# Kernel tuning notes

Measured on AMD Instinct MI355X. Metric: run time of the kernel, lower is better.

## Reference

```python
import jax, jax.numpy as jnp
import numpy as np

N_NODES = 100000
N_EDGES = 3200000
IN_DIM = 4
HID = 128
OUT_DIM = 4


def setup_inputs() -> dict:
    key = jax.random.key(0)
    ks = jax.random.split(key, 16)
    x = jax.random.normal(ks[0], (N_NODES, IN_DIM), dtype=jnp.float32)
    edge_index = jax.random.randint(ks[1], (2, N_EDGES), 0, N_NODES, dtype=jnp.int32)
    hidden_mask = jax.random.randint(ks[2], (N_NODES,), 0, 2) > 0
    def glorot(k, shape):
        fan_in, fan_out = shape[0], shape[1]
        s = jnp.sqrt(6.0 / (fan_in + fan_out))
        return jax.random.uniform(k, shape, jnp.float32, -s, s)
    return {
        "x": x,
        "edge_index": edge_index,
        "hidden_mask": hidden_mask,
        "W0": glorot(ks[3], (IN_DIM, HID)), "b0": jnp.zeros((HID,), jnp.float32),
        "res_W": glorot(ks[4], (IN_DIM, HID)), "res_b": jnp.zeros((HID,), jnp.float32),
        "W1": glorot(ks[5], (HID, HID)), "b1": jnp.zeros((HID,), jnp.float32),
        "W2": glorot(ks[6], (HID, HID)), "b2": jnp.zeros((HID,), jnp.float32),
        "fc_W": glorot(ks[7], (HID, OUT_DIM)), "fc_b": jnp.zeros((OUT_DIM,), jnp.float32),
    }


def _gcn_norm(edge_index, num_nodes):
    # add self loops, compute symmetric normalization (PyG GCNConv default)
    loop = jnp.arange(num_nodes, dtype=edge_index.dtype)
    src = jnp.concatenate([edge_index[0], loop])
    dst = jnp.concatenate([edge_index[1], loop])
    deg = jax.ops.segment_sum(jnp.ones_like(dst, dtype=jnp.float32), dst,
                              num_segments=num_nodes)
    dis = jnp.where(deg > 0, jax.lax.rsqrt(deg), 0.0)  # deg^{-1/2}, inf -> 0
    norm = dis[src] * dis[dst]  # [E + N]
    return src, dst, norm


def _gcn_conv(h, W, b, src, dst, norm, num_nodes):
    h = h @ W                       # [N, out]
    msg = h[src] * norm[:, None]    # gather + scale, [E+N, out]
    agg = jax.ops.segment_sum(msg, dst, num_segments=num_nodes)
    return agg + b


def reference(x, edge_index, hidden_mask, W0, b0, res_W, res_b, W1, b1, W2, b2, fc_W, fc_b):
    n = x.shape[0]
    src, dst, norm = _gcn_norm(edge_index, n)
    # mask input features (mask broadcast over 4 feature cols)
    h = jnp.where(hidden_mask[:, None], x, 0.0)
    # layer 0: in_dim != hidden -> linear residual
    out0 = _gcn_conv(h, W0, b0, src, dst, norm, n)
    h = jax.nn.relu(out0 + (h @ res_W + res_b))
    # layers 1,2: identity residual
    h = jax.nn.relu(_gcn_conv(h, W1, b1, src, dst, norm, n) + h)
    h = jax.nn.relu(_gcn_conv(h, W2, b2, src, dst, norm, n) + h)
    x_out = h @ fc_W + fc_b
    return (x_out, hidden_mask)
```

## Files before the change

### kernel.cpp

```cpp
#include <hip/hip_runtime.h>
#include <hip/hip_bf16.h>
#include <stdint.h>

#define HID 128
#define NPART 8
#define NCHUNK 256
#define MCHUNK 4096
#define LBITS 10
#define SBITS 22

__global__ void detect_mask_kernel(const unsigned char* __restrict__ p, int nbytes,
                                   int nfloat, int* __restrict__ flags) {
  int stride = blockDim.x * gridDim.x;
  for (int i = blockIdx.x * blockDim.x + threadIdx.x; i < nbytes; i += stride) {
    if ((i & 3) && p[i] != 0) { atomicOr(&flags[0], 1); break; }
  }
  const float* fp = (const float*)p;
  for (int i = blockIdx.x * blockDim.x + threadIdx.x; i < nfloat; i += stride) {
    float f = fp[i];
    if (!(f == 0.0f || f == 1.0f)) { atomicOr(&flags[1], 1); break; }
  }
}

__global__ void expand_mask_h0(const void* __restrict__ maskp, const float4* __restrict__ x4,
                               const int* __restrict__ flags, const float* __restrict__ dis,
                               float* __restrict__ maskout, float* __restrict__ cvec,
                               float4* __restrict__ h0s, int N) {
  int i = blockIdx.x * blockDim.x + threadIdx.x;
  if (i >= N) return;
  float m;
  if (flags[0] == 0)      m = (((const int*)maskp)[i] != 0) ? 1.f : 0.f;
  else if (flags[1] == 0) m = (((const float*)maskp)[i] != 0.f) ? 1.f : 0.f;
  else                    m = (((const unsigned char*)maskp)[i] != 0) ? 1.f : 0.f;
  maskout[i] = m;
  float4 xv = x4[i];
  float4 h0 = make_float4(m * xv.x, m * xv.y, m * xv.z, m * xv.w);
  float* cv = cvec + (size_t)i * 8;
  cv[4] = h0.x; cv[5] = h0.y; cv[6] = h0.z; cv[7] = h0.w;
  float d = dis[i];
  h0s[i] = make_float4(d * h0.x, d * h0.y, d * h0.z, d * h0.w);
}

__global__ void init_gcur_kernel(int* __restrict__ gcur, int n, int CAPB) {
  int i = blockIdx.x * blockDim.x + threadIdx.x;
  if (i < n) gcur[i] = i * CAPB;
}

__global__ void radixA_kernel(const int* __restrict__ src, const int* __restrict__ dst,
                              int* __restrict__ gcur, uint32_t* __restrict__ bdata,
                              int nbin, int CAPB, int E) {
  __shared__ uint32_t sv[MCHUNK];
  __shared__ uint16_t sb[MCHUNK];
  __shared__ int bcnt[1024], boff[1024], gbase[1024];
  __shared__ int wsum[4];
  int t = threadIdx.x;
  int base = blockIdx.x * MCHUNK;
  int m = E - base; if (m > MCHUNK) m = MCHUNK;
  for (int i = t; i < 1024; i += 256) bcnt[i] = 0;
  __syncthreads();
  uint32_t pk[16]; short bn[16];
#pragma unroll
  for (int j = 0; j < 16; j++) {
    int i = base + t + j * 256;
    if (i < base + m) {
      int d = __builtin_nontemporal_load(&dst[i]);
      int s = __builtin_nontemporal_load(&src[i]);
      int b = d >> LBITS;
      pk[j] = ((uint32_t)(d & ((1 << LBITS) - 1)) << SBITS) | (uint32_t)s;
      bn[j] = (short)b;
      atomicAdd(&bcnt[b], 1);
    } else bn[j] = -1;
  }
  __syncthreads();
  {
    int lane = t & 63, w = t >> 6, i0 = t * 4;
    int v0 = bcnt[i0], v1 = bcnt[i0 + 1], v2 = bcnt[i0 + 2], v3 = bcnt[i0 + 3];
    int ts = v0 + v1 + v2 + v3, sc = ts;
    for (int d = 1; d < 64; d <<= 1) { int x = __shfl_up(sc, d, 64); if (lane >= d) sc += x; }
    if (lane == 63) wsum[w] = sc;
    __syncthreads();
    int wo = 0;
    for (int k = 0; k < w; k++) wo += wsum[k];
    int excl = wo + sc - ts;
    boff[i0] = excl; boff[i0 + 1] = excl + v0;
    boff[i0 + 2] = excl + v0 + v1; boff[i0 + 3] = excl + v0 + v1 + v2;
  }
  __syncthreads();
  for (int i = t; i < nbin; i += 256) {
    int c = bcnt[i];
    gbase[i] = c ? atomicAdd(&gcur[i], c) : 0;
  }
  __syncthreads();
  for (int i = t; i < nbin; i += 256) bcnt[i] = boff[i];
  __syncthreads();
#pragma unroll
  for (int j = 0; j < 16; j++) {
    if (bn[j] >= 0) {
      int p = atomicAdd(&bcnt[bn[j]], 1);
      sv[p] = pk[j];
      sb[p] = (uint16_t)bn[j];
    }
  }
  __syncthreads();
  for (int i = t; i < m; i += 256) {
    int b = sb[i];
    int gp = gbase[b] + (i - boff[b]);
    if (gp < (b + 1) * CAPB) bdata[gp] = sv[i];
  }
}

__global__ void bucket_meta_kernel(const int* __restrict__ gcur, int* __restrict__ bstart,
                                   int nbin, int CAPB) {
  __shared__ int wsum[4];
  int t = threadIdx.x, lane = t & 63, w = t >> 6, i0 = t * 4;
  int v[4];
#pragma unroll
  for (int q = 0; q < 4; q++) {
    int i = i0 + q;
    int c = 0;
    if (i < nbin) {
      c = gcur[i] - i * CAPB;
      if (c > CAPB) c = CAPB;
    }
    v[q] = c;
  }
  int ts = v[0] + v[1] + v[2] + v[3], sc = ts;
  for (int d = 1; d < 64; d <<= 1) { int x = __shfl_up(sc, d, 64); if (lane >= d) sc += x; }
  if (lane == 63) wsum[w] = sc;
  __syncthreads();
  int wo = 0;
  for (int k = 0; k < w; k++) wo += wsum[k];
  int excl = wo + sc - ts;
  int e[4] = {excl, excl + v[0], excl + v[0] + v[1], excl + v[0] + v[1] + v[2]};
#pragma unroll
  for (int q = 0; q < 4; q++)
    if (i0 + q < nbin) bstart[i0 + q] = e[q];
  if (t == 255) bstart[nbin] = wo + sc;
}

__global__ void radixB_kernel(const uint32_t* __restrict__ bdata, const int* __restrict__ gcur,
                              const int* __restrict__ bstart, int CAPB,
                              int* __restrict__ off, float* __restrict__ dis,
                              int* __restrict__ csr, int N, int E) {
  __shared__ int cnt[1024], loff[1024];
  __shared__ int wsum[4];
  int b = blockIdx.x, t = threadIdx.x;
  int cb = gcur[b] - b * CAPB; if (cb > CAPB) cb = CAPB;
  int gb = bstart[b];
  const uint32_t* bd = bdata + (size_t)b * CAPB;
  for (int i = t; i < 1024; i += 256) cnt[i] = 0;
  __syncthreads();
  for (int i = t; i < cb; i += 256) atomicAdd(&cnt[bd[i] >> SBITS], 1);
  __syncthreads();
  {
    int lane = t & 63, w = t >> 6, i0 = t * 4;
    int v0 = cnt[i0], v1 = cnt[i0 + 1], v2 = cnt[i0 + 2], v3 = cnt[i0 + 3];
    int ts = v0 + v1 + v2 + v3, sc = ts;
    for (int d = 1; d < 64; d <<= 1) { int x = __shfl_up(sc, d, 64); if (lane >= d) sc += x; }
    if (lane == 63) wsum[w] = sc;
    __syncthreads();
    int wo = 0;
    for (int k = 0; k < w; k++) wo += wsum[k];
    int e0 = wo + sc - ts;
    int e1 = e0 + v0, e2 = e1 + v1, e3 = e2 + v2;
    loff[i0] = e0; loff[i0 + 1] = e1; loff[i0 + 2] = e2; loff[i0 + 3] = e3;
    int d0 = b * 1024 + i0;
    if (d0 + 0 < N) { off[d0 + 0] = gb + e0; dis[d0 + 0] = rsqrtf((float)v0 + 1.0f); }
    if (d0 + 1 < N) { off[d0 + 1] = gb + e1; dis[d0 + 1] = rsqrtf((float)v1 + 1.0f); }
    if (d0 + 2 < N) { off[d0 + 2] = gb + e2; dis[d0 + 2] = rsqrtf((float)v2 + 1.0f); }
    if (d0 + 3 < N) { off[d0 + 3] = gb + e3; dis[d0 + 3] = rsqrtf((float)v3 + 1.0f); }
  }
  if (b == 0 && t == 0) off[N] = E;
  __syncthreads();
  for (int i = t; i < 1024; i += 256) cnt[i] = loff[i];
  __syncthreads();
  for (int i = t; i < cb; i += 256) {
    uint32_t v = bd[i];
    int p = atomicAdd(&cnt[v >> SBITS], 1);
    csr[gb + p] = (int)(v & ((1u << SBITS) - 1));
  }
}

__global__ void scan1_kernel(const int* __restrict__ cnt, int* __restrict__ off,
                             int* __restrict__ bsum, float* __restrict__ dis, int N) {
  __shared__ int wsum[4];
  int t = threadIdx.x, lane = t & 63, w = t >> 6;
  int base = blockIdx.x * 1024 + t * 4;
  int v0 = (base + 0 < N) ? cnt[base + 0] : 0;
  int v1 = (base + 1 < N) ? cnt[base + 1] : 0;
  int v2 = (base + 2 < N) ? cnt[base + 2] : 0;
  int v3 = (base + 3 < N) ? cnt[base + 3] : 0;
  if (dis) {
    if (base + 0 < N) dis[base + 0] = rsqrtf((float)v0 + 1.0f);
    if (base + 1 < N) dis[base + 1] = rsqrtf((float)v1 + 1.0f);
    if (base + 2 < N) dis[base + 2] = rsqrtf((float)v2 + 1.0f);
    if (base + 3 < N) dis[base + 3] = rsqrtf((float)v3 + 1.0f);
  }
  int ts = v0 + v1 + v2 + v3;
  int sc = ts;
  for (int d = 1; d < 64; d <<= 1) {
    int x = __shfl_up(sc, d, 64);
    if (lane >= d) sc += x;
  }
  if (lane == 63) wsum[w] = sc;
  __syncthreads();
  int wo = 0;
  for (int i = 0; i < w; i++) wo += wsum[i];
  int excl = wo + sc - ts;
  if (base + 0 < N) off[base + 0] = excl;
  if (base + 1 < N) off[base + 1] = excl + v0;
  if (base + 2 < N) off[base + 2] = excl + v0 + v1;
  if (base + 3 < N) off[base + 3] = excl + v0 + v1 + v2;
  if (t == 255) bsum[blockIdx.x] = wo + sc;
}

__global__ void scan2_kernel(int* __restrict__ bsum, int nb) {
  if (threadIdx.x == 0 && blockIdx.x == 0) {
    int run = 0;
    for (int i = 0; i < nb; i++) { int v = bsum[i]; bsum[i] = run; run += v; }
  }
}

__global__ void scan3_kernel(int* __restrict__ off, const int* __restrict__ bsum,
                             int* __restrict__ cur, int N, int E) {
  int i = blockIdx.x * blockDim.x + threadIdx.x;
  if (i < N) {
    int o = off[i] + bsum[i >> 10];
    off[i] = o;
    if (cur) cur[i] = o;
  }
  if (i == 0) off[N] = E;
}

__global__ void hist_part_kernel(const int* __restrict__ dst, int* __restrict__ cnt,
                                 int E, int N) {
  int p = blockIdx.x & (NPART - 1);
  int chunk = blockIdx.x >> 3;
  int lo = (int)((long long)p * N / NPART);
  int hi = (int)((long long)(p + 1) * N / NPART);
  int stride = NCHUNK * 256;
  for (int e = chunk * 256 + threadIdx.x; e < E; e += stride) {
    int d = __builtin_nontemporal_load(&dst[e]);
    if (d >= lo && d < hi) atomicAdd(&cnt[d], 1);
  }
}

__global__ void fill_part_kernel(const int* __restrict__ src, const int* __restrict__ dst,
                                 int* __restrict__ cur, int* __restrict__ csr, int E, int N) {
  int p = blockIdx.x & (NPART - 1);
  int chunk = blockIdx.x >> 3;
  int lo = (int)((long long)p * N / NPART);
  int hi = (int)((long long)(p + 1) * N / NPART);
  int stride = NCHUNK * 256;
  for (int e = chunk * 256 + threadIdx.x; e < E; e += stride) {
    int d = __builtin_nontemporal_load(&dst[e]);
    if (d >= lo && d < hi) {
      int s = __builtin_nontemporal_load(&src[e]);
      int pos = atomicAdd(&cur[d], 1);
      csr[pos] = s;
    }
  }
}

__global__ void l0_agg_kernel(const float4* __restrict__ h0s, const float* __restrict__ dis,
                              const int* __restrict__ off, const int* __restrict__ csr,
                              float* __restrict__ cvec, int N) {
  int n = blockIdx.x * blockDim.x + threadIdx.x;
  if (n >= N) return;
  float4 a = h0s[n];
  int e0 = off[n], e1 = off[n + 1];
  int i = e0;
  for (; i < e1 && (i & 3); i++) {
    float4 v = h0s[csr[i]];
    a.x += v.x; a.y += v.y; a.z += v.z; a.w += v.w;
  }
  for (; i + 4 <= e1; i += 4) {
    int4 c = *(const int4*)&csr[i];
    float4 v0 = h0s[c.x], v1 = h0s[c.y], v2 = h0s[c.z], v3 = h0s[c.w];
    a.x += v0.x + v1.x + v2.x + v3.x;
    a.y += v0.y + v1.y + v2.y + v3.y;
    a.z += v0.z + v1.z + v2.z + v3.z;
    a.w += v0.w + v1.w + v2.w + v3.w;
  }
  for (; i < e1; i++) {
    float4 v = h0s[csr[i]];
    a.x += v.x; a.y += v.y; a.z += v.z; a.w += v.w;
  }
  float dn = dis[n];
  float* cv = cvec + (size_t)n * 8;
  cv[0] = dn * a.x; cv[1] = dn * a.y; cv[2] = dn * a.z; cv[3] = dn * a.w;
}

__global__ void l0_combine_kernel(const float* __restrict__ cvec, const float* __restrict__ W0,
                                  const float* __restrict__ b0, const float* __restrict__ resW,
                                  const float* __restrict__ resb, const float* __restrict__ dis,
                                  float* __restrict__ h1, __hip_bfloat16* __restrict__ hbout) {
  int idx = blockIdx.x * blockDim.x + threadIdx.x;
  int n = idx >> 7, c = idx & 127;
  const float* cv = cvec + (size_t)n * 8;
  float acc = b0[c] + resb[c];
#pragma unroll
  for (int k = 0; k < 4; k++) {
    acc += cv[k] * W0[k * HID + c];
    acc += cv[4 + k] * resW[k * HID + c];
  }
  float v = fmaxf(acc, 0.0f);
  h1[idx] = v;
  if (hbout) hbout[idx] = __float2bfloat16(dis[n] * v);
}

#define ACC1(W) { a0 += __uint_as_float((W) << 16); a1 += __uint_as_float((W) & 0xffff0000u); }
__global__ void agg_hid_bf16_kernel(const uint32_t* __restrict__ hb, const float* __restrict__ dis,
                                    const int* __restrict__ off, const int* __restrict__ csr,
                                    uint32_t* __restrict__ aggout, int N) {
  int node = blockIdx.x * 4 + (threadIdx.x >> 6);
  int lane = threadIdx.x & 63;
  if (node >= N) return;
  uint32_t w = hb[(size_t)node * 64 + lane];
  float a0 = __uint_as_float(w << 16);
  float a1 = __uint_as_float(w & 0xffff0000u);
  int e0 = off[node], e1 = off[node + 1];
  int i = e0;
  for (; i < e1 && (i & 3); i++) {
    uint32_t ww = hb[(size_t)csr[i] * 64 + lane];
    ACC1(ww)
  }
  for (; i + 8 <= e1; i += 8) {
    int4 c0 = *(const int4*)&csr[i];
    int4 c1 = *(const int4*)&csr[i + 4];
    uint32_t w0 = hb[(size_t)c0.x * 64 + lane];
    uint32_t w1 = hb[(size_t)c0.y * 64 + lane];
    uint32_t w2 = hb[(size_t)c0.z * 64 + lane];
    uint32_t w3 = hb[(size_t)c0.w * 64 + lane];
    uint32_t w4 = hb[(size_t)c1.x * 64 + lane];
    uint32_t w5 = hb[(size_t)c1.y * 64 + lane];
    uint32_t w6 = hb[(size_t)c1.z * 64 + lane];
    uint32_t w7 = hb[(size_t)c1.w * 64 + lane];
    ACC1(w0) ACC1(w1) ACC1(w2) ACC1(w3) ACC1(w4) ACC1(w5) ACC1(w6) ACC1(w7)
  }
  for (; i + 4 <= e1; i += 4) {
    int4 c = *(const int4*)&csr[i];
    uint32_t w0 = hb[(size_t)c.x * 64 + lane];
    uint32_t w1 = hb[(size_t)c.y * 64 + lane];
    uint32_t w2 = hb[(size_t)c.z * 64 + lane];
    uint32_t w3 = hb[(size_t)c.w * 64 + lane];
    ACC1(w0) ACC1(w1) ACC1(w2) ACC1(w3)
  }
  for (; i < e1; i++) {
    uint32_t ww = hb[(size_t)csr[i] * 64 + lane];
    ACC1(ww)
  }
  float dn = dis[node];
  __hip_bfloat162 p = __float22bfloat162_rn(make_float2(dn * a0, dn * a1));
  aggout[(size_t)node * 64 + lane] = *(uint32_t*)&p;
}

__global__ void agg_hid_kernel(const float* __restrict__ h, const float* __restrict__ dis,
                               const int* __restrict__ off, const int* __restrict__ csr,
                               float* __restrict__ out, int N) {
  int node = blockIdx.x * 4 + (threadIdx.x >> 6);
  int lane = threadIdx.x & 63;
  if (node >= N) return;
  float dn = dis[node];
  const float* hrow = h + (size_t)node * HID;
  float a0 = dn * hrow[lane];
  float a1 = dn * hrow[lane + 64];
  int e0 = off[node], e1 = off[node + 1];
  for (int i = e0; i < e1; i++) {
    int s = csr[i];
    float d = dis[s];
    const float* hs = h + (size_t)s * HID;
    a0 += d * hs[lane];
    a1 += d * hs[lane + 64];
  }
  out[(size_t)node * HID + lane] = dn * a0;
  out[(size_t)node * HID + lane + 64] = dn * a1;
}

__global__ void gemm_resid_relu_kernel(const void* __restrict__ agp, int agBf16,
                                       float* __restrict__ hout,
                                       const float* __restrict__ hres,
                                       const float* __restrict__ W, const float* __restrict__ b,
                                       const float* __restrict__ dis,
                                       __hip_bfloat16* __restrict__ hbout, int N) {
  __shared__ float ash[64 * HID];
  int t = threadIdx.x;
  int n0 = blockIdx.x * 64;
  if (agBf16) {
    const uint32_t* agb = (const uint32_t*)agp;
    for (int i = t; i < 64 * 64; i += 256) {
      int gn = n0 + (i >> 6);
      uint32_t w = (gn < N) ? agb[(size_t)gn * 64 + (i & 63)] : 0u;
      ash[(i >> 6) * HID + (i & 63) * 2]     = __uint_as_float(w << 16);
      ash[(i >> 6) * HID + (i & 63) * 2 + 1] = __uint_as_float(w & 0xffff0000u);
    }
  } else {
    const float* agf = (const float*)agp;
    for (int i = t; i < 64 * HID; i += 256) {
      int gn = n0 + (i >> 7);
      ash[i] = (gn < N) ? agf[(size_t)gn * HID + (i & 127)] : 0.0f;
    }
  }
  __syncthreads();
  int tc = t & 31;
  int tn = t >> 5;
  float acc[8][4];
#pragma unroll
  for (int j = 0; j < 8; j++)
#pragma unroll
    for (int q = 0; q < 4; q++) acc[j][q] = 0.0f;

  for (int k = 0; k < HID; k += 4) {
    float4 w0 = *(const float4*)&W[(k + 0) * HID + tc * 4];
    float4 w1 = *(const float4*)&W[(k + 1) * HID + tc * 4];
    float4 w2 = *(const float4*)&W[(k + 2) * HID + tc * 4];
    float4 w3 = *(const float4*)&W[(k + 3) * HID + tc * 4];
#pragma unroll
    for (int j = 0; j < 8; j++) {
      float4 a = *(const float4*)&ash[(tn * 8 + j) * HID + k];
      acc[j][0] += a.x * w0.x + a.y * w1.x + a.z * w2.x + a.w * w3.x;
      acc[j][1] += a.x * w0.y + a.y * w1.y + a.z * w2.y + a.w * w3.y;
      acc[j][2] += a.x * w0.z + a.y * w1.z + a.z * w2.z + a.w * w3.z;
      acc[j][3] += a.x * w0.w + a.y * w1.w + a.z * w2.w + a.w * w3.w;
    }
  }
  float4 bv = *(const float4*)&b[tc * 4];
#pragma unroll
  for (int j = 0; j < 8; j++) {
    int gn = n0 + tn * 8 + j;
    if (gn < N) {
      float4 hv = *(const float4*)&hres[(size_t)gn * HID + tc * 4];
      float4 o;
      o.x = fmaxf(acc[j][0] + bv.x + hv.x, 0.0f);
      o.y = fmaxf(acc[j][1] + bv.y + hv.y, 0.0f);
      o.z = fmaxf(acc[j][2] + bv.z + hv.z, 0.0f);
      o.w = fmaxf(acc[j][3] + bv.w + hv.w, 0.0f);
      *(float4*)&hout[(size_t)gn * HID + tc * 4] = o;
      if (hbout) {
        float dnn = dis[gn];
        __hip_bfloat162 p01 = __float22bfloat162_rn(make_float2(dnn * o.x, dnn * o.y));
        __hip_bfloat162 p23 = __float22bfloat162_rn(make_float2(dnn * o.z, dnn * o.w));
        *(__hip_bfloat162*)&hbout[(size_t)gn * HID + tc * 4] = p01;
        *(__hip_bfloat162*)&hbout[(size_t)gn * HID + tc * 4 + 2] = p23;
      }
    }
  }
}

__global__ void gemm_resid_fc_kernel(const void* __restrict__ agp, int agBf16,
                                     const float* __restrict__ hres,
                                     const float* __restrict__ W, const float* __restrict__ b,
                                     const float* __restrict__ fcW, const float* __restrict__ fcb,
                                     float* __restrict__ out, int N) {
  __shared__ float ash[64 * HID];
  int t = threadIdx.x;
  int n0 = blockIdx.x * 64;
  if (agBf16) {
    const uint32_t* agb = (const uint32_t*)agp;
    for (int i = t; i < 64 * 64; i += 256) {
      int gn = n0 + (i >> 6);
      uint32_t w = (gn < N) ? agb[(size_t)gn * 64 + (i & 63)] : 0u;
      ash[(i >> 6) * HID + (i & 63) * 2]     = __uint_as_float(w << 16);
      ash[(i >> 6) * HID + (i & 63) * 2 + 1] = __uint_as_float(w & 0xffff0000u);
    }
  } else {
    const float* agf = (const float*)agp;
    for (int i = t; i < 64 * HID; i += 256) {
      int gn = n0 + (i >> 7);
      ash[i] = (gn < N) ? agf[(size_t)gn * HID + (i & 127)] : 0.0f;
    }
  }
  __syncthreads();
  int tc = t & 31;
  int tn = t >> 5;
  float acc[8][4];
#pragma unroll
  for (int j = 0; j < 8; j++)
#pragma unroll
    for (int q = 0; q < 4; q++) acc[j][q] = 0.0f;

  for (int k = 0; k < HID; k += 4) {
    float4 w0 = *(const float4*)&W[(k + 0) * HID + tc * 4];
    float4 w1 = *(const float4*)&W[(k + 1) * HID + tc * 4];
    float4 w2 = *(const float4*)&W[(k + 2) * HID + tc * 4];
    float4 w3 = *(const float4*)&W[(k + 3) * HID + tc * 4];
#pragma unroll
    for (int j = 0; j < 8; j++) {
      float4 a = *(const float4*)&ash[(tn * 8 + j) * HID + k];
      acc[j][0] += a.x * w0.x + a.y * w1.x + a.z * w2.x + a.w * w3.x;
      acc[j][1] += a.x * w0.y + a.y * w1.y + a.z * w2.y + a.w * w3.y;
      acc[j][2] += a.x * w0.z + a.y * w1.z + a.z * w2.z + a.w * w3.z;
      acc[j][3] += a.x * w0.w + a.y * w1.w + a.z * w2.w + a.w * w3.w;
    }
  }
  float4 f0 = *(const float4*)&fcW[(tc * 4 + 0) * 4];
  float4 f1 = *(const float4*)&fcW[(tc * 4 + 1) * 4];
  float4 f2 = *(const float4*)&fcW[(tc * 4 + 2) * 4];
  float4 f3 = *(const float4*)&fcW[(tc * 4 + 3) * 4];
  float4 bv = *(const float4*)&b[tc * 4];
  float4 fb = *(const float4*)&fcb[0];
#pragma unroll
  for (int j = 0; j < 8; j++) {
    int gn = n0 + tn * 8 + j;
    float4 o = make_float4(0.f, 0.f, 0.f, 0.f);
    if (gn < N) {
      float4 hv = *(const float4*)&hres[(size_t)gn * HID + tc * 4];
      o.x = fmaxf(acc[j][0] + bv.x + hv.x, 0.0f);
      o.y = fmaxf(acc[j][1] + bv.y + hv.y, 0.0f);
      o.z = fmaxf(acc[j][2] + bv.z + hv.z, 0.0f);
      o.w = fmaxf(acc[j][3] + bv.w + hv.w, 0.0f);
    }
    float r0 = o.x * f0.x + o.y * f1.x + o.z * f2.x + o.w * f3.x;
    float r1 = o.x * f0.y + o.y * f1.y + o.z * f2.y + o.w * f3.y;
    float r2 = o.x * f0.z + o.y * f1.z + o.z * f2.z + o.w * f3.z;
    float r3 = o.x * f0.w + o.y * f1.w + o.z * f2.w + o.w * f3.w;
#pragma unroll
    for (int d = 1; d < 32; d <<= 1) {
      r0 += __shfl_xor(r0, d, 64);
      r1 += __shfl_xor(r1, d, 64);
      r2 += __shfl_xor(r2, d, 64);
      r3 += __shfl_xor(r3, d, 64);
    }
    if (tc == 0 && gn < N)
      *(float4*)&out[(size_t)gn * 4] =
          make_float4(r0 + fb.x, r1 + fb.y, r2 + fb.z, r3 + fb.w);
  }
}

extern "C" void kernel_launch(void* const* d_in, const int* in_sizes, int n_in,
                              void* d_out, int out_size, void* d_ws, size_t ws_size,
                              hipStream_t stream) {
  const float* x = (const float*)d_in[0];
  const int* edge = (const int*)d_in[1];
  const void* maskp = d_in[2];
  const float* W0 = (const float*)d_in[3];
  const float* b0 = (const float*)d_in[4];
  const float* resW = (const float*)d_in[5];
  const float* resb = (const float*)d_in[6];
  const float* W1 = (const float*)d_in[7];
  const float* b1 = (const float*)d_in[8];
  const float* W2 = (const float*)d_in[9];
  const float* b2 = (const float*)d_in[10];
  const float* fcW = (const float*)d_in[11];
  const float* fcb = (const float*)d_in[12];
  float* out = (float*)d_out;

  int N = in_sizes[0] / 4;
  int E = in_sizes[1] / 2;
  const int* srcp = edge;
  const int* dstp = edge + E;

  char* ws = (char*)d_ws;
  size_t cursor = 0;
  auto alloc = [&](size_t bytes) { char* p = ws + cursor; cursor += (bytes + 511) & ~(size_t)511; return p; };
  int* flags = (int*)alloc(16);
  int* cnt = (int*)alloc((size_t)N * 4);
  float* dis = (float*)alloc((size_t)N * 4);
  int* off = (int*)alloc((size_t)(N + 1) * 4);
  int* bsum = (int*)alloc(1024);
  int nbin = (N + 1023) >> 10;
  int* gcur = (int*)alloc((size_t)(nbin + 1) * 4);
  int* bstart = (int*)alloc((size_t)(nbin + 1) * 4);
  int* csr = (int*)alloc((size_t)E * 4);
  float* h0s = (float*)alloc((size_t)N * 4 * 4);
  float* cvec = (float*)alloc((size_t)N * 8 * 4);
  float* buf0 = (float*)alloc((size_t)N * HID * 4);
  float* buf1 = (float*)alloc((size_t)N * HID * 4);
  size_t base_cursor = cursor;
  __hip_bfloat16* hb = (__hip_bfloat16*)alloc((size_t)N * HID * 2);
  uint32_t* aggbf = (uint32_t*)alloc((size_t)N * 64 * 4);
  bool use_bf16 = (cursor <= ws_size);
  if (!use_bf16) {
    hb = nullptr;
    aggbf = nullptr;
    if (base_cursor > ws_size) return;
  }

  long long expect = (long long)E / (nbin > 0 ? nbin : 1);
  int CAPB = (int)((((expect * 5) / 4 + 127) / 64) * 64);
  if (CAPB < 256) CAPB = 256;
  size_t bdata_bytes = (size_t)nbin * CAPB * 4;
  bool use_radix = (N <= (1 << SBITS)) && (nbin <= 1024) &&
                   (bdata_bytes <= (size_t)N * HID * 4);
  uint32_t* bdata = (uint32_t*)buf1;

  int nThreadsN = (N + 255) / 256;

  hipMemsetAsync(flags, 0, 16, stream);
  detect_mask_kernel<<<256, 256, 0, stream>>>((const unsigned char*)maskp, N, N / 4, flags);

  if (use_radix) {
    init_gcur_kernel<<<(nbin + 255) / 256, 256, 0, stream>>>(gcur, nbin, CAPB);
    radixA_kernel<<<(E + MCHUNK - 1) / MCHUNK, 256, 0, stream>>>(srcp, dstp, gcur, bdata,
                                                                 nbin, CAPB, E);
    bucket_meta_kernel<<<1, 256, 0, stream>>>(gcur, bstart, nbin, CAPB);
    radixB_kernel<<<nbin, 256, 0, stream>>>(bdata, gcur, bstart, CAPB, off, dis, csr, N, E);
  } else {
    hipMemsetAsync(cnt, 0, (size_t)N * 4, stream);
    int nb = (N + 1023) / 1024;
    hist_part_kernel<<<NPART * NCHUNK, 256, 0, stream>>>(dstp, cnt, E, N);
    scan1_kernel<<<nb, 256, 0, stream>>>(cnt, off, bsum, dis, N);
    scan2_kernel<<<1, 64, 0, stream>>>(bsum, nb);
    scan3_kernel<<<nThreadsN, 256, 0, stream>>>(off, bsum, cnt, N, E);
    fill_part_kernel<<<NPART * NCHUNK, 256, 0, stream>>>(srcp, dstp, cnt, csr, E, N);
  }

  expand_mask_h0<<<nThreadsN, 256, 0, stream>>>(maskp, (const float4*)x, flags, dis,
                                                out + (size_t)N * 4, cvec, (float4*)h0s, N);

  l0_agg_kernel<<<nThreadsN, 256, 0, stream>>>((const float4*)h0s, dis, off, csr, cvec, N);
  l0_combine_kernel<<<(N * HID + 255) / 256, 256, 0, stream>>>(cvec, W0, b0, resW, resb, dis,
                                                               buf0, hb);

  if (use_bf16) {
    agg_hid_bf16_kernel<<<(N + 3) / 4, 256, 0, stream>>>((const uint32_t*)hb, dis, off, csr,
                                                         aggbf, N);
    gemm_resid_relu_kernel<<<(N + 63) / 64, 256, 0, stream>>>(aggbf, 1, buf1, buf0, W1, b1,
                                                              dis, hb, N);
    agg_hid_bf16_kernel<<<(N + 3) / 4, 256, 0, stream>>>((const uint32_t*)hb, dis, off, csr,
                                                         aggbf, N);
    gemm_resid_fc_kernel<<<(N + 63) / 64, 256, 0, stream>>>(aggbf, 1, buf1, W2, b2,
                                                            fcW, fcb, out, N);
  } else {
    agg_hid_kernel<<<(N + 3) / 4, 256, 0, stream>>>(buf0, dis, off, csr, buf1, N);
    gemm_resid_relu_kernel<<<(N + 63) / 64, 256, 0, stream>>>(buf1, 0, buf1, buf0, W1, b1,
                                                              dis, nullptr, N);
    agg_hid_kernel<<<(N + 3) / 4, 256, 0, stream>>>(buf1, dis, off, csr, buf0, N);
    gemm_resid_fc_kernel<<<(N + 63) / 64, 256, 0, stream>>>(buf0, 0, buf1, W2, b2,
                                                            fcW, fcb, out, N);
  }
}
```

Baseline: 539.0 us.

## Fuse neighbor aggregation into hidden-layer GEMM kernels via shared-memory tile

The separate bf16 aggregation kernel and the following GEMM kernel for layers 1 and 2 are merged. Each 64-node block gathers its neighbor sums directly into shared memory in fp32, then runs the dense transform, residual and ReLU (plus the fc projection in the last layer). This removes the intermediate aggregate buffer round-trip and one launch per layer. It uses separate ping-pong bf16 buffers to avoid read/write races. The gather loop is unrolled to 16 edges. The cost is that each block now does both a latency-bound gather and compute, with only 4 waves per 64 nodes doing the gather, so there is less parallelism for latency hiding.

```diff
diff --git a/kernel.cpp b/kernel.cpp
--- a/kernel.cpp
+++ b/kernel.cpp
@@ -310,49 +310,188 @@
 }
 
 #define ACC1(W) { a0 += __uint_as_float((W) << 16); a1 += __uint_as_float((W) & 0xffff0000u); }
-__global__ void agg_hid_bf16_kernel(const uint32_t* __restrict__ hb, const float* __restrict__ dis,
-                                    const int* __restrict__ off, const int* __restrict__ csr,
-                                    uint32_t* __restrict__ aggout, int N) {
-  int node = blockIdx.x * 4 + (threadIdx.x >> 6);
-  int lane = threadIdx.x & 63;
-  if (node >= N) return;
-  uint32_t w = hb[(size_t)node * 64 + lane];
-  float a0 = __uint_as_float(w << 16);
-  float a1 = __uint_as_float(w & 0xffff0000u);
-  int e0 = off[node], e1 = off[node + 1];
-  int i = e0;
-  for (; i < e1 && (i & 3); i++) {
-    uint32_t ww = hb[(size_t)csr[i] * 64 + lane];
-    ACC1(ww)
-  }
-  for (; i + 8 <= e1; i += 8) {
-    int4 c0 = *(const int4*)&csr[i];
-    int4 c1 = *(const int4*)&csr[i + 4];
-    uint32_t w0 = hb[(size_t)c0.x * 64 + lane];
-    uint32_t w1 = hb[(size_t)c0.y * 64 + lane];
-    uint32_t w2 = hb[(size_t)c0.z * 64 + lane];
-    uint32_t w3 = hb[(size_t)c0.w * 64 + lane];
-    uint32_t w4 = hb[(size_t)c1.x * 64 + lane];
-    uint32_t w5 = hb[(size_t)c1.y * 64 + lane];
-    uint32_t w6 = hb[(size_t)c1.z * 64 + lane];
-    uint32_t w7 = hb[(size_t)c1.w * 64 + lane];
-    ACC1(w0) ACC1(w1) ACC1(w2) ACC1(w3) ACC1(w4) ACC1(w5) ACC1(w6) ACC1(w7)
-  }
-  for (; i + 4 <= e1; i += 4) {
-    int4 c = *(const int4*)&csr[i];
-    uint32_t w0 = hb[(size_t)c.x * 64 + lane];
-    uint32_t w1 = hb[(size_t)c.y * 64 + lane];
-    uint32_t w2 = hb[(size_t)c.z * 64 + lane];
-    uint32_t w3 = hb[(size_t)c.w * 64 + lane];
-    ACC1(w0) ACC1(w1) ACC1(w2) ACC1(w3)
-  }
-  for (; i < e1; i++) {
-    uint32_t ww = hb[(size_t)csr[i] * 64 + lane];
-    ACC1(ww)
-  }
-  float dn = dis[node];
-  __hip_bfloat162 p = __float22bfloat162_rn(make_float2(dn * a0, dn * a1));
-  aggout[(size_t)node * 64 + lane] = *(uint32_t*)&p;
+
+__device__ __forceinline__ void gather_tile(const uint32_t* __restrict__ hb,
+                                            const float* __restrict__ dis,
+                                            const int* __restrict__ off,
+                                            const int* __restrict__ csr,
+                                            float* __restrict__ ash, int n0, int N) {
+  int t = threadIdx.x, lane = t & 63, wv = t >> 6;
+  for (int ln = wv * 16; ln < wv * 16 + 16; ln++) {
+    int node = n0 + ln;
+    float a0 = 0.f, a1 = 0.f;
+    if (node < N) {
+      uint32_t w = hb[(size_t)node * 64 + lane];
+      a0 = __uint_as_float(w << 16);
+      a1 = __uint_as_float(w & 0xffff0000u);
+      int e0 = off[node], e1 = off[node + 1];
+      int i = e0;
+      for (; i < e1 && (i & 3); i++) {
+        uint32_t ww = hb[(size_t)csr[i] * 64 + lane];
+        ACC1(ww)
+      }
+      for (; i + 16 <= e1; i += 16) {
+        int4 c0 = *(const int4*)&csr[i];
+        int4 c1 = *(const int4*)&csr[i + 4];
+        int4 c2 = *(const int4*)&csr[i + 8];
+        int4 c3 = *(const int4*)&csr[i + 12];
+        uint32_t w0 = hb[(size_t)c0.x * 64 + lane];
+        uint32_t w1 = hb[(size_t)c0.y * 64 + lane];
+        uint32_t w2 = hb[(size_t)c0.z * 64 + lane];
+        uint32_t w3 = hb[(size_t)c0.w * 64 + lane];
+        uint32_t w4 = hb[(size_t)c1.x * 64 + lane];
+        uint32_t w5 = hb[(size_t)c1.y * 64 + lane];
+        uint32_t w6 = hb[(size_t)c1.z * 64 + lane];
+        uint32_t w7 = hb[(size_t)c1.w * 64 + lane];
+        uint32_t w8 = hb[(size_t)c2.x * 64 + lane];
+        uint32_t w9 = hb[(size_t)c2.y * 64 + lane];
+        uint32_t wa = hb[(size_t)c2.z * 64 + lane];
+        uint32_t wb = hb[(size_t)c2.w * 64 + lane];
+        uint32_t wc = hb[(size_t)c3.x * 64 + lane];
+        uint32_t wd = hb[(size_t)c3.y * 64 + lane];
+        uint32_t we = hb[(size_t)c3.z * 64 + lane];
+        uint32_t wf = hb[(size_t)c3.w * 64 + lane];
+        ACC1(w0) ACC1(w1) ACC1(w2) ACC1(w3) ACC1(w4) ACC1(w5) ACC1(w6) ACC1(w7)
+        ACC1(w8) ACC1(w9) ACC1(wa) ACC1(wb) ACC1(wc) ACC1(wd) ACC1(we) ACC1(wf)
+      }
+      for (; i + 4 <= e1; i += 4) {
+        int4 c = *(const int4*)&csr[i];
+        uint32_t w0 = hb[(size_t)c.x * 64 + lane];
+        uint32_t w1 = hb[(size_t)c.y * 64 + lane];
+        uint32_t w2 = hb[(size_t)c.z * 64 + lane];
+        uint32_t w3 = hb[(size_t)c.w * 64 + lane];
+        ACC1(w0) ACC1(w1) ACC1(w2) ACC1(w3)
+      }
+      for (; i < e1; i++) {
+        uint32_t ww = hb[(size_t)csr[i] * 64 + lane];
+        ACC1(ww)
+      }
+      float dn = dis[node];
+      a0 *= dn; a1 *= dn;
+    }
+    *(float2*)&ash[ln * HID + 2 * lane] = make_float2(a0, a1);
+  }
+}
+
+__global__ void agg_gemm_kernel(const uint32_t* __restrict__ hb, const float* __restrict__ dis,
+                                const int* __restrict__ off, const int* __restrict__ csr,
+                                const float* __restrict__ hres,
+                                const float* __restrict__ W, const float* __restrict__ b,
+                                float* __restrict__ hout, __hip_bfloat16* __restrict__ hbout,
+                                int N) {
+  __shared__ float ash[64 * HID];
+  int t = threadIdx.x;
+  int n0 = blockIdx.x * 64;
+  gather_tile(hb, dis, off, csr, ash, n0, N);
+  __syncthreads();
+  int tc = t & 31;
+  int tn = t >> 5;
+  float acc[8][4];
+#pragma unroll
+  for (int j = 0; j < 8; j++)
+#pragma unroll
+    for (int q = 0; q < 4; q++) acc[j][q] = 0.0f;
+
+  for (int k = 0; k < HID; k += 4) {
+    float4 w0 = *(const float4*)&W[(k + 0) * HID + tc * 4];
+    float4 w1 = *(const float4*)&W[(k + 1) * HID + tc * 4];
+    float4 w2 = *(const float4*)&W[(k + 2) * HID + tc * 4];
+    float4 w3 = *(const float4*)&W[(k + 3) * HID + tc * 4];
+#pragma unroll
+    for (int j = 0; j < 8; j++) {
+      float4 a = *(const float4*)&ash[(tn * 8 + j) * HID + k];
+      acc[j][0] += a.x * w0.x + a.y * w1.x + a.z * w2.x + a.w * w3.x;
+      acc[j][1] += a.x * w0.y + a.y * w1.y + a.z * w2.y + a.w * w3.y;
+      acc[j][2] += a.x * w0.z + a.y * w1.z + a.z * w2.z + a.w * w3.z;
+      acc[j][3] += a.x * w0.w + a.y * w1.w + a.z * w2.w + a.w * w3.w;
+    }
+  }
+  float4 bv = *(const float4*)&b[tc * 4];
+#pragma unroll
+  for (int j = 0; j < 8; j++) {
+    int gn = n0 + tn * 8 + j;
+    if (gn < N) {
+      float4 hv = *(const float4*)&hres[(size_t)gn * HID + tc * 4];
+      float4 o;
+      o.x = fmaxf(acc[j][0] + bv.x + hv.x, 0.0f);
+      o.y = fmaxf(acc[j][1] + bv.y + hv.y, 0.0f);
+      o.z = fmaxf(acc[j][2] + bv.z + hv.z, 0.0f);
+      o.w = fmaxf(acc[j][3] + bv.w + hv.w, 0.0f);
+      *(float4*)&hout[(size_t)gn * HID + tc * 4] = o;
+      float dnn = dis[gn];
+      __hip_bfloat162 p01 = __float22bfloat162_rn(make_float2(dnn * o.x, dnn * o.y));
+      __hip_bfloat162 p23 = __float22bfloat162_rn(make_float2(dnn * o.z, dnn * o.w));
+      *(__hip_bfloat162*)&hbout[(size_t)gn * HID + tc * 4] = p01;
+      *(__hip_bfloat162*)&hbout[(size_t)gn * HID + tc * 4 + 2] = p23;
+    }
+  }
+}
+
+__global__ void agg_gemm_fc_kernel(const uint32_t* __restrict__ hb, const float* __restrict__ dis,
+                                   const int* __restrict__ off, const int* __restrict__ csr,
+                                   const float* __restrict__ hres,
+                                   const float* __restrict__ W, const float* __restrict__ b,
+                                   const float* __restrict__ fcW, const float* __restrict__ fcb,
+                                   float* __restrict__ out, int N) {
+  __shared__ float ash[64 * HID];
+  int t = threadIdx.x;
+  int n0 = blockIdx.x * 64;
+  gather_tile(hb, dis, off, csr, ash, n0, N);
+  __syncthreads();
+  int tc = t & 31;
+  int tn = t >> 5;
+  float acc[8][4];
+#pragma unroll
+  for (int j = 0; j < 8; j++)
+#pragma unroll
+    for (int q = 0; q < 4; q++) acc[j][q] = 0.0f;
+
+  for (int k = 0; k < HID; k += 4) {
+    float4 w0 = *(const float4*)&W[(k + 0) * HID + tc * 4];
+    float4 w1 = *(const float4*)&W[(k + 1) * HID + tc * 4];
+    float4 w2 = *(const float4*)&W[(k + 2) * HID + tc * 4];
+    float4 w3 = *(const float4*)&W[(k + 3) * HID + tc * 4];
+#pragma unroll
+    for (int j = 0; j < 8; j++) {
+      float4 a = *(const float4*)&ash[(tn * 8 + j) * HID + k];
+      acc[j][0] += a.x * w0.x + a.y * w1.x + a.z * w2.x + a.w * w3.x;
+      acc[j][1] += a.x * w0.y + a.y * w1.y + a.z * w2.y + a.w * w3.y;
+      acc[j][2] += a.x * w0.z + a.y * w1.z + a.z * w2.z + a.w * w3.z;
+      acc[j][3] += a.x * w0.w + a.y * w1.w + a.z * w2.w + a.w * w3.w;
+    }
+  }
+  float4 f0 = *(const float4*)&fcW[(tc * 4 + 0) * 4];
+  float4 f1 = *(const float4*)&fcW[(tc * 4 + 1) * 4];
+  float4 f2 = *(const float4*)&fcW[(tc * 4 + 2) * 4];
+  float4 f3 = *(const float4*)&fcW[(tc * 4 + 3) * 4];
+  float4 bv = *(const float4*)&b[tc * 4];
+  float4 fb = *(const float4*)&fcb[0];
+#pragma unroll
+  for (int j = 0; j < 8; j++) {
+    int gn = n0 + tn * 8 + j;
+    float4 o = make_float4(0.f, 0.f, 0.f, 0.f);
+    if (gn < N) {
+      float4 hv = *(const float4*)&hres[(size_t)gn * HID + tc * 4];
+      o.x = fmaxf(acc[j][0] + bv.x + hv.x, 0.0f);
+      o.y = fmaxf(acc[j][1] + bv.y + hv.y, 0.0f);
+      o.z = fmaxf(acc[j][2] + bv.z + hv.z, 0.0f);
+      o.w = fmaxf(acc[j][3] + bv.w + hv.w, 0.0f);
+    }
+    float r0 = o.x * f0.x + o.y * f1.x + o.z * f2.x + o.w * f3.x;
+    float r1 = o.x * f0.y + o.y * f1.y + o.z * f2.y + o.w * f3.y;
+    float r2 = o.x * f0.z + o.y * f1.z + o.z * f2.z + o.w * f3.z;
+    float r3 = o.x * f0.w + o.y * f1.w + o.z * f2.w + o.w * f3.w;
+#pragma unroll
+    for (int d = 1; d < 32; d <<= 1) {
+      r0 += __shfl_xor(r0, d, 64);
+      r1 += __shfl_xor(r1, d, 64);
+      r2 += __shfl_xor(r2, d, 64);
+      r3 += __shfl_xor(r3, d, 64);
+    }
+    if (tc == 0 && gn < N)
+      *(float4*)&out[(size_t)gn * 4] =
+          make_float4(r0 + fb.x, r1 + fb.y, r2 + fb.z, r3 + fb.w);
+  }
 }
 
 __global__ void agg_hid_kernel(const float* __restrict__ h, const float* __restrict__ dis,
@@ -377,29 +516,16 @@
   out[(size_t)node * HID + lane + 64] = dn * a1;
 }
 
-__global__ void gemm_resid_relu_kernel(const void* __restrict__ agp, int agBf16,
-                                       float* __restrict__ hout,
+__global__ void gemm_resid_relu_kernel(const float* __restrict__ ag, float* __restrict__ hout,
                                        const float* __restrict__ hres,
                                        const float* __restrict__ W, const float* __restrict__ b,
-                                       const float* __restrict__ dis,
-                                       __hip_bfloat16* __restrict__ hbout, int N) {
+                                       int N) {
   __shared__ float ash[64 * HID];
   int t = threadIdx.x;
   int n0 = blockIdx.x * 64;
-  if (agBf16) {
-    const uint32_t* agb = (const uint32_t*)agp;
-    for (int i = t; i < 64 * 64; i += 256) {
-      int gn = n0 + (i >> 6);
-      uint32_t w = (gn < N) ? agb[(size_t)gn * 64 + (i & 63)] : 0u;
-      ash[(i >> 6) * HID + (i & 63) * 2]     = __uint_as_float(w << 16);
-      ash[(i >> 6) * HID + (i & 63) * 2 + 1] = __uint_as_float(w & 0xffff0000u);
-    }
-  } else {
-    const float* agf = (const float*)agp;
-    for (int i = t; i < 64 * HID; i += 256) {
-      int gn = n0 + (i >> 7);
-      ash[i] = (gn < N) ? agf[(size_t)gn * HID + (i & 127)] : 0.0f;
-    }
+  for (int i = t; i < 64 * HID; i += 256) {
+    int gn = n0 + (i >> 7);
+    ash[i] = (gn < N) ? ag[(size_t)gn * HID + (i & 127)] : 0.0f;
   }
   __syncthreads();
   int tc = t & 31;
@@ -409,7 +535,6 @@
   for (int j = 0; j < 8; j++)
 #pragma unroll
     for (int q = 0; q < 4; q++) acc[j][q] = 0.0f;
-
   for (int k = 0; k < HID; k += 4) {
     float4 w0 = *(const float4*)&W[(k + 0) * HID + tc * 4];
     float4 w1 = *(const float4*)&W[(k + 1) * HID + tc * 4];
@@ -436,18 +561,11 @@
       o.z = fmaxf(acc[j][2] + bv.z + hv.z, 0.0f);
       o.w = fmaxf(acc[j][3] + bv.w + hv.w, 0.0f);
       *(float4*)&hout[(size_t)gn * HID + tc * 4] = o;
-      if (hbout) {
-        float dnn = dis[gn];
-        __hip_bfloat162 p01 = __float22bfloat162_rn(make_float2(dnn * o.x, dnn * o.y));
-        __hip_bfloat162 p23 = __float22bfloat162_rn(make_float2(dnn * o.z, dnn * o.w));
-        *(__hip_bfloat162*)&hbout[(size_t)gn * HID + tc * 4] = p01;
-        *(__hip_bfloat162*)&hbout[(size_t)gn * HID + tc * 4 + 2] = p23;
-      }
-    }
-  }
-}
-
-__global__ void gemm_resid_fc_kernel(const void* __restrict__ agp, int agBf16,
+    }
+  }
+}
+
+__global__ void gemm_resid_fc_kernel(const float* __restrict__ ag,
                                      const float* __restrict__ hres,
                                      const float* __restrict__ W, const float* __restrict__ b,
                                      const float* __restrict__ fcW, const float* __restrict__ fcb,
@@ -455,20 +573,9 @@
   __shared__ float ash[64 * HID];
   int t = threadIdx.x;
   int n0 = blockIdx.x * 64;
-  if (agBf16) {
-    const uint32_t* agb = (const uint32_t*)agp;
-    for (int i = t; i < 64 * 64; i += 256) {
-      int gn = n0 + (i >> 6);
-      uint32_t w = (gn < N) ? agb[(size_t)gn * 64 + (i & 63)] : 0u;
-      ash[(i >> 6) * HID + (i & 63) * 2]     = __uint_as_float(w << 16);
-      ash[(i >> 6) * HID + (i & 63) * 2 + 1] = __uint_as_float(w & 0xffff0000u);
-    }
-  } else {
-    const float* agf = (const float*)agp;
-    for (int i = t; i < 64 * HID; i += 256) {
-      int gn = n0 + (i >> 7);
-      ash[i] = (gn < N) ? agf[(size_t)gn * HID + (i & 127)] : 0.0f;
-    }
+  for (int i = t; i < 64 * HID; i += 256) {
+    int gn = n0 + (i >> 7);
+    ash[i] = (gn < N) ? ag[(size_t)gn * HID + (i & 127)] : 0.0f;
   }
   __syncthreads();
   int tc = t & 31;
@@ -478,7 +585,6 @@
   for (int j = 0; j < 8; j++)
 #pragma unroll
     for (int q = 0; q < 4; q++) acc[j][q] = 0.0f;
-
   for (int k = 0; k < HID; k += 4) {
     float4 w0 = *(const float4*)&W[(k + 0) * HID + tc * 4];
     float4 w1 = *(const float4*)&W[(k + 1) * HID + tc * 4];
@@ -567,12 +673,11 @@
   float* buf0 = (float*)alloc((size_t)N * HID * 4);
   float* buf1 = (float*)alloc((size_t)N * HID * 4);
   size_t base_cursor = cursor;
-  __hip_bfloat16* hb = (__hip_bfloat16*)alloc((size_t)N * HID * 2);
-  uint32_t* aggbf = (uint32_t*)alloc((size_t)N * 64 * 4);
+  __hip_bfloat16* hb1 = (__hip_bfloat16*)alloc((size_t)N * HID * 2);
+  __hip_bfloat16* hb2 = (__hip_bfloat16*)alloc((size_t)N * HID * 2);
   bool use_bf16 = (cursor <= ws_size);
   if (!use_bf16) {
-    hb = nullptr;
-    aggbf = nullptr;
+    hb1 = nullptr; hb2 = nullptr;
     if (base_cursor > ws_size) return;
   }
 
@@ -585,6 +690,7 @@
   uint32_t* bdata = (uint32_t*)buf1;
 
   int nThreadsN = (N + 255) / 256;
+  int ngemm = (N + 63) / 64;
 
   hipMemsetAsync(flags, 0, 16, stream);
   detect_mask_kernel<<<256, 256, 0, stream>>>((const unsigned char*)maskp, N, N / 4, flags);
@@ -610,23 +716,17 @@
 
   l0_agg_kernel<<<nThreadsN, 256, 0, stream>>>((const float4*)h0s, dis, off, csr, cvec, N);
   l0_combine_kernel<<<(N * HID + 255) / 256, 256, 0, stream>>>(cvec, W0, b0, resW, resb, dis,
-                                                               buf0, hb);
+                                                               buf0, hb1);
 
   if (use_bf16) {
-    agg_hid_bf16_kernel<<<(N + 3) / 4, 256, 0, stream>>>((const uint32_t*)hb, dis, off, csr,
-                                                         aggbf, N);
-    gemm_resid_relu_kernel<<<(N + 63) / 64, 256, 0, stream>>>(aggbf, 1, buf1, buf0, W1, b1,
-                                                              dis, hb, N);
-    agg_hid_bf16_kernel<<<(N + 3) / 4, 256, 0, stream>>>((const uint32_t*)hb, dis, off, csr,
-                                                         aggbf, N);
-    gemm_resid_fc_kernel<<<(N + 63) / 64, 256, 0, stream>>>(aggbf, 1, buf1, W2, b2,
-                                                            fcW, fcb, out, N);
+    agg_gemm_kernel<<<ngemm, 256, 0, stream>>>((const uint32_t*)hb1, dis, off, csr,
+                                               buf0, W1, b1, buf1, hb2, N);
+    agg_gemm_fc_kernel<<<ngemm, 256, 0, stream>>>((const uint32_t*)hb2, dis, off, csr,
+                                                  buf1, W2, b2, fcW, fcb, out, N);
   } else {
     agg_hid_kernel<<<(N + 3) / 4, 256, 0, stream>>>(buf0, dis, off, csr, buf1, N);
-    gemm_resid_relu_kernel<<<(N + 63) / 64, 256, 0, stream>>>(buf1, 0, buf1, buf0, W1, b1,
-                                                              dis, nullptr, N);
+    gemm_resid_relu_kernel<<<ngemm, 256, 0, stream>>>(buf1, buf1, buf0, W1, b1, N);
     agg_hid_kernel<<<(N + 3) / 4, 256, 0, stream>>>(buf1, dis, off, csr, buf0, N);
-    gemm_resid_fc_kernel<<<(N + 63) / 64, 256, 0, stream>>>(buf0, 0, buf1, W2, b2,
-                                                            fcW, fcb, out, N);
-  }
-}
+    gemm_resid_fc_kernel<<<ngemm, 256, 0, stream>>>(buf0, buf1, W2, b2, fcW, fcb, out, N);
+  }
+}
```

Measured after the change: 612.6 us. 13.6% more time.
